# Performance work log

Measured on AMD Instinct MI355X. Metric: run time of the kernel, lower is better.

Reference implementation:

```python
import jax, jax.numpy as jnp
import numpy as np

R = 45        # num_dep_rels
L = 384       # sent_len
D = 512       # word representation dim = in_size*2
E_REL = 15    # dep_rel_emb_size
IN4 = 1024    # in_size*4
HOPS = 3
THRESH = 1e-06


def setup_inputs() -> dict:
    key = jax.random.key(0)
    ks = jax.random.split(key, 10)
    energy = jax.random.uniform(ks[0], (1, R, L, L), dtype=jnp.float32)
    word_h = jax.random.normal(ks[1], (1, L, D), dtype=jnp.float32)
    e1 = jax.random.normal(ks[2], (D,), dtype=jnp.float32)
    e2 = jax.random.normal(ks[3], (D,), dtype=jnp.float32)
    # learned params
    rel_embs = jax.random.normal(ks[4], (R, E_REL), dtype=jnp.float32)
    Wc = jax.random.normal(ks[5], (2 * D + E_REL, D), dtype=jnp.float32) * 0.02
    bc = jnp.zeros((D,), dtype=jnp.float32)
    Wk = jax.random.normal(ks[6], (HOPS, IN4, IN4), dtype=jnp.float32) * 0.02
    bk = jnp.zeros((HOPS, IN4), dtype=jnp.float32)
    Wh = jax.random.normal(ks[7], (HOPS, IN4, IN4), dtype=jnp.float32) * 0.02
    bh = jnp.zeros((HOPS, IN4), dtype=jnp.float32)
    return {"energy": energy, "word_h": word_h, "e1": e1, "e2": e2,
            "sent_len": L, "rel_embs": rel_embs, "Wc": Wc, "bc": bc,
            "Wk": Wk, "bk": bk, "Wh": Wh, "bh": bh}


def reference(energy, word_h, e1, e2, sent_len, rel_embs, Wc, bc, Wk, bk, Wh, bh):
    Ls = sent_len
    E = energy[0, :, :Ls, :Ls]                 # [R, L, L]
    marg = E.sum(axis=0)                       # [L, L] marginal energy
    # threshold back-off (try t, t/10, t/100 until some arc survives)
    m0 = marg > THRESH
    m1 = marg > THRESH * 0.1
    m2 = marg > THRESH * 0.01
    mask = jnp.where(m0.any(), m0, jnp.where(m1.any(), m1, m2))  # [L, L]

    H = word_h[0, :Ls]                         # [L, D]
    w = marg.reshape(-1)                       # [L*L] arc weights
    # rel embedding per arc: sum_r E[r,h,d] * rel_embs[r,e]
    rels = jnp.einsum('rhd,re->hde', E, rel_embs).reshape(Ls * Ls, E_REL)
    head_t = jnp.repeat(H, Ls, axis=0) * w[:, None]   # [L*L, D]
    dep_t = jnp.tile(H, (Ls, 1)) * w[:, None]         # [L*L, D]
    arc_in = jnp.concatenate([head_t, rels, dep_t], axis=1)  # [L*L, 2D+15]
    mem_bank = jax.nn.leaky_relu(arc_in @ Wc + bc)    # [L*L, D] (dropout=eval)
    maskf = mask.reshape(-1)                          # [L*L]

    # multi-hop memory attention; filtered-out arcs get zero attention weight
    inputs = jnp.concatenate([e1, e2])                # [1024]
    for i in range(HOPS):
        kv = inputs @ Wk[i] + bk[i]                   # [1024]
        k_, v_ = jnp.split(kv, 2)                     # chunk along dim 0
        k_ = jnp.tanh(k_)
        v_ = jax.nn.leaky_relu(v_)
        scores = jnp.where(maskf, mem_bank @ k_, -1e30)  # [L*L]
        dist = jax.nn.softmax(scores)
        mem_rep = dist @ mem_bank                     # [D]
        inputs = jax.nn.leaky_relu(jnp.concatenate([v_, mem_rep]) @ Wh[i] + bh[i])
    return inputs
```

## Files before the change

### kernel.cpp

```cpp
#include <hip/hip_runtime.h>
#include <hip/hip_bf16.h>
#include <cstdint>
#include <cstddef>

#define LL      147456
#define NBLK    768
#define CHB     12
#define NPACK   288

typedef __attribute__((ext_vector_type(8))) short  short8;
typedef __attribute__((ext_vector_type(4))) float  f32x4;

#define EPACK_OFF   0u
#define MARG_OFF    14155776u
#define A_OFF       14745600u
#define BTC_OFF     15532032u
#define UTGP_OFF    16318464u
#define XIN_OFF     16367616u
#define KBUF_OFF    16371712u
#define VBUF_OFF    16373760u
#define MEMREP_OFF  16375808u
#define PM_OFF      16377856u
#define PL_OFF      16380928u
#define SRAW_OFF    16384000u
#define BLKF_OFF    16973824u

#define SKIP_LD     20.0f

static __device__ __forceinline__ ushort f2bf(float x) {
  uint u = __float_as_uint(x);
  return (ushort)((u + 0x7fffu + ((u >> 16) & 1u)) >> 16);
}
static __device__ __forceinline__ float lrelu(float x) { return fmaxf(x, 0.01f * x); }

__global__ __launch_bounds__(256) void k_prep(
    const float* __restrict__ E, uint4* __restrict__ ep,
    float* __restrict__ marg, int* __restrict__ blkflags,
    const float* __restrict__ H, const float* __restrict__ Wc,
    const float* __restrict__ rel, const float* __restrict__ bc,
    float* __restrict__ A, float* __restrict__ Btc, uint4* __restrict__ Utgp) {
  __shared__ float Hs[4][512];
  __shared__ float Ps[4][512];
  __shared__ int fsh;
  int b = blockIdx.x, t = threadIdx.x;
  if (b < 192) {
    bool roleA = (b < 96);
    int g0 = (roleA ? b : b - 96) * 4;
    const float* Wcp = Wc + (size_t)(roleA ? 0 : 527) * 512;
    for (int i = t; i < 4 * 512; i += 256) Hs[i >> 9][i & 511] = H[(size_t)g0 * 512 + i];
    __syncthreads();
    int cq = t & 127, q = t >> 7;
    int c0 = cq * 4;
    f32x4 acc[4];
#pragma unroll
    for (int i = 0; i < 4; ++i) acc[i] = (f32x4){0.f, 0.f, 0.f, 0.f};
    for (int k = q * 256; k < q * 256 + 256; ++k) {
      f32x4 wv = *(const f32x4*)&Wcp[(size_t)k * 512 + c0];
#pragma unroll
      for (int i = 0; i < 4; ++i) { float hv = Hs[i][k]; acc[i] += hv * wv; }
    }
    if (q == 1) {
#pragma unroll
      for (int i = 0; i < 4; ++i) *(f32x4*)&Ps[i][c0] = acc[i];
    }
    __syncthreads();
    if (q == 0) {
#pragma unroll
      for (int i = 0; i < 4; ++i) {
        acc[i] += *(const f32x4*)&Ps[i][c0];
        if (roleA) {
          *(f32x4*)&A[(size_t)(g0 + i) * 512 + c0] = acc[i];
        } else {
#pragma unroll
          for (int j = 0; j < 4; ++j) Btc[(size_t)(c0 + j) * 384 + (g0 + i)] = acc[i][j];
        }
      }
    }
  } else if (b == 192) {
    for (int c = t; c < 512; c += 256) {
      float uv[48];
#pragma unroll
      for (int k = 0; k < 45; ++k) {
        float s = 0.f;
#pragma unroll
        for (int e = 0; e < 15; ++e) s += rel[k * 15 + e] * Wc[(size_t)(512 + e) * 512 + c];
        uv[k] = s;
      }
      uv[45] = bc[c]; uv[46] = 0.f; uv[47] = 0.f;
#pragma unroll
      for (int g = 0; g < 6; ++g) {
        uint w[4];
#pragma unroll
        for (int p = 0; p < 4; ++p)
          w[p] = (uint)f2bf(uv[g * 8 + 2 * p]) | ((uint)f2bf(uv[g * 8 + 2 * p + 1]) << 16);
        uint4 v; v.x = w[0]; v.y = w[1]; v.z = w[2]; v.w = w[3];
        Utgp[g * 512 + c] = v;
      }
    }
  } else {
    if (t == 0) fsh = 0;
    int bp = b - 193;
    size_t hd0 = (size_t)bp * 512 + 2 * t;
    float2 ev[46];
#pragma unroll
    for (int r = 0; r < 45; ++r) ev[r] = *(const float2*)&E[(size_t)r * LL + hd0];
    ev[45] = make_float2(1.0f, 1.0f);
    float s0 = 0.f, s1 = 0.f;
#pragma unroll
    for (int r = 0; r < 45; ++r) { s0 += ev[r].x; s1 += ev[r].y; }
#pragma unroll
    for (int o = 0; o < 6; ++o) {
      uint wa[4], wb[4];
#pragma unroll
      for (int p = 0; p < 4; ++p) {
        int r0 = 8 * o + 2 * p, r1 = r0 + 1;
        float a0 = (r0 < 46) ? ev[r0].x : 0.f, a1 = (r1 < 46) ? ev[r1].x : 0.f;
        float b0 = (r0 < 46) ? ev[r0].y : 0.f, b1 = (r1 < 46) ? ev[r1].y : 0.f;
        wa[p] = (uint)f2bf(a0) | ((uint)f2bf(a1) << 16);
        wb[p] = (uint)f2bf(b0) | ((uint)f2bf(b1) << 16);
      }
      uint4 va; va.x = wa[0]; va.y = wa[1]; va.z = wa[2]; va.w = wa[3];
      uint4 vb; vb.x = wb[0]; vb.y = wb[1]; vb.z = wb[2]; vb.w = wb[3];
      ep[(size_t)o * LL + hd0] = va;
      ep[(size_t)o * LL + hd0 + 1] = vb;
    }
    *(float2*)&marg[hd0] = make_float2(s0, s1);
    int f = (s0 > 1e-6f ? 1 : 0) | (s0 > 1e-7f ? 2 : 0) | (s0 > 1e-8f ? 4 : 0)
          | (s1 > 1e-6f ? 1 : 0) | (s1 > 1e-7f ? 2 : 0) | (s1 > 1e-8f ? 4 : 0);
#pragma unroll
    for (int d = 1; d < 64; d <<= 1) f |= __shfl_xor(f, d);
    __syncthreads();
    if ((t & 63) == 0) atomicOr(&fsh, f);
    __syncthreads();
    if (t == 0) blkflags[bp] = fsh;
  }
}

__global__ __launch_bounds__(256) void k_gemv(const float* __restrict__ W, const float* __restrict__ bias,
                                              const float* __restrict__ xA, const float* __restrict__ xB,
                                              float* __restrict__ outA, float* __restrict__ outB,
                                              float* __restrict__ out2, int mode) {
  __shared__ float xs[1024];
  __shared__ float red[8][32];
  int t = threadIdx.x;
  for (int i = t; i < 1024; i += 256) xs[i] = (i < 512) ? xA[i] : xB[i - 512];
  __syncthreads();
  int jj = t & 31, kq = t >> 5;
  int j = blockIdx.x * 32 + jj;
  float acc = 0.f;
#pragma unroll 8
  for (int k = kq * 128; k < kq * 128 + 128; ++k) acc = fmaf(xs[k], W[(size_t)k * 1024 + j], acc);
  red[kq][jj] = acc;
  __syncthreads();
  if (kq == 0) {
    float s = bias[j];
#pragma unroll
    for (int q = 0; q < 8; ++q) s += red[q][jj];
    if (mode == 0) {
      if (j < 512) outA[j] = tanhf(s);
      else outB[j - 512] = lrelu(s);
    } else {
      float rv = lrelu(s);
      outA[j] = rv;
      if (out2) out2[j] = rv;
    }
  }
}

__global__ __launch_bounds__(256, 3) void k_scores(
    const uint4* __restrict__ ep, const float* __restrict__ marg,
    const float* __restrict__ A, const float* __restrict__ Btc,
    const uint4* __restrict__ Utgp, const int* __restrict__ blkflags,
    const float* __restrict__ kvec,
    float* __restrict__ pm, float* __restrict__ pl, float* __restrict__ sraw,
    float* __restrict__ memrep) {
  __shared__ __align__(16) uint4 uthF[6 * 512];
  __shared__ float sbuf[CHB * 16];
  __shared__ float redw[8];
  __shared__ int fsh;
  int t = threadIdx.x, b = blockIdx.x;
  int dbt = b >> 5, hg = b & 31;
  int dbase = dbt * 16, h0 = hg * CHB;
  int lane = t & 63, wid = t >> 6;
  int l15 = lane & 15, qq = lane >> 4;

  if (b == 0) { memrep[t] = 0.f; memrep[t + 256] = 0.f; }
  if (t == 0) fsh = 0;
  for (int i = t; i < 6 * 512; i += 256) uthF[i] = Utgp[i];
  int f = 0;
  for (int i = t; i < NPACK; i += 256) f |= blkflags[i];
#pragma unroll
  for (int d = 1; d < 64; d <<= 1) f |= __shfl_xor(f, d);

  const short8 zero8 = (short8){0, 0, 0, 0, 0, 0, 0, 0};
  short8 a0[3], a1[3];
  f32x4 wq[3];
#pragma unroll
  for (int k3 = 0; k3 < 3; ++k3) {
    int h = h0 + wid * 3 + k3;
    int hda = h * 384 + dbase + l15;
    uint4 r0 = ep[(size_t)qq * LL + hda];
    a0[k3] = *(short8*)&r0;
    if (qq < 2) { uint4 r1 = ep[(size_t)(4 + qq) * LL + hda]; a1[k3] = *(short8*)&r1; }
    else a1[k3] = zero8;
    wq[k3] = *(const f32x4*)&marg[h * 384 + dbase + qq * 4];
  }
  __syncthreads();
  if ((t & 63) == 0) atomicOr(&fsh, f);

  float sp[3][4];
#pragma unroll
  for (int k3 = 0; k3 < 3; ++k3)
#pragma unroll
    for (int j = 0; j < 4; ++j) sp[k3][j] = 0.f;

  for (int half = 0; half < 2; ++half) {
    float kreg[16];
#pragma unroll
    for (int tt = 0; tt < 16; ++tt) kreg[tt] = kvec[half * 256 + tt * 16 + l15];
#pragma unroll 4
    for (int tt = 0; tt < 16; ++tt) {
      int c = half * 256 + tt * 16 + l15;
      short8 b0 = *(short8*)&uthF[qq * 512 + c];
      short8 b1 = (qq < 2) ? *(short8*)&uthF[(4 + qq) * 512 + c] : zero8;
      f32x4 btv = *(const f32x4*)&Btc[(size_t)c * 384 + dbase + qq * 4];
      const float* Ap = &A[(size_t)(h0 + wid * 3) * 512 + c];
      float av[3]; av[0] = Ap[0]; av[1] = Ap[512]; av[2] = Ap[1024];
#pragma unroll
      for (int k3 = 0; k3 < 3; ++k3) {
        f32x4 cc = (f32x4){0.f, 0.f, 0.f, 0.f};
        cc = __builtin_amdgcn_mfma_f32_16x16x32_bf16(a0[k3], b0, cc, 0, 0, 0);
        cc = __builtin_amdgcn_mfma_f32_16x16x32_bf16(a1[k3], b1, cc, 0, 0, 0);
        float aw = av[k3];
        float x0 = cc[0] + wq[k3][0] * (aw + btv[0]); float mb0 = fmaxf(x0, 0.01f * x0);
        float x1 = cc[1] + wq[k3][1] * (aw + btv[1]); float mb1 = fmaxf(x1, 0.01f * x1);
        float x2 = cc[2] + wq[k3][2] * (aw + btv[2]); float mb2 = fmaxf(x2, 0.01f * x2);
        float x3 = cc[3] + wq[k3][3] * (aw + btv[3]); float mb3 = fmaxf(x3, 0.01f * x3);
        sp[k3][0] = fmaf(mb0, kreg[tt], sp[k3][0]);
        sp[k3][1] = fmaf(mb1, kreg[tt], sp[k3][1]);
        sp[k3][2] = fmaf(mb2, kreg[tt], sp[k3][2]);
        sp[k3][3] = fmaf(mb3, kreg[tt], sp[k3][3]);
      }
    }
  }
#pragma unroll
  for (int k3 = 0; k3 < 3; ++k3)
#pragma unroll
    for (int j = 0; j < 4; ++j) {
#pragma unroll
      for (int d = 1; d < 16; d <<= 1) sp[k3][j] += __shfl_xor(sp[k3][j], d);
    }
  __syncthreads();
  float thr = (fsh & 1) ? 1e-6f : ((fsh & 2) ? 1e-7f : 1e-8f);
  if (l15 == 0) {
#pragma unroll
    for (int k3 = 0; k3 < 3; ++k3) {
      int base = (wid * 3 + k3) * 16 + qq * 4;
#pragma unroll
      for (int j = 0; j < 4; ++j)
        sbuf[base + j] = (wq[k3][j] > thr) ? sp[k3][j] : -1e30f;
    }
  }
  __syncthreads();
  float s = (t < CHB * 16) ? sbuf[t] : -1e30f;
  float m = s;
#pragma unroll
  for (int d = 1; d < 64; d <<= 1) m = fmaxf(m, __shfl_xor(m, d));
  if (lane == 0) redw[wid] = m;
  __syncthreads();
  float mloc = fmaxf(fmaxf(redw[0], redw[1]), fmaxf(redw[2], redw[3]));
  float e = (t < CHB * 16) ? __expf(s - mloc) : 0.f;
#pragma unroll
  for (int d = 1; d < 64; d <<= 1) e += __shfl_xor(e, d);
  if (lane == 0) redw[4 + wid] = e;
  if (t < CHB * 16) sraw[(size_t)b * 192 + t] = s;
  __syncthreads();
  if (t == 0) { pm[b] = mloc; pl[b] = redw[4] + redw[5] + redw[6] + redw[7]; }
}

__global__ __launch_bounds__(256, 3) void k_pv(
    const uint4* __restrict__ ep, const float* __restrict__ marg,
    const float* __restrict__ A, const float* __restrict__ Btc,
    const uint4* __restrict__ Utgp, const float* __restrict__ pm,
    const float* __restrict__ pl, const float* __restrict__ sraw,
    float* __restrict__ memrep) {
  __shared__ __align__(16) uint4 uthF[6 * 512];
  __shared__ float pbuf[CHB * 16];
  __shared__ float paccs[256];
  __shared__ float redm[8];
  int t = threadIdx.x, b = blockIdx.x;
  int lane = t & 63, wid = t >> 6;

  float m = -1e30f;
  for (int i = t; i < NBLK; i += 256) m = fmaxf(m, pm[i]);
#pragma unroll
  for (int d = 1; d < 64; d <<= 1) m = fmaxf(m, __shfl_xor(m, d));
  if (lane == 0) redm[wid] = m;
  __syncthreads();
  float M = fmaxf(fmaxf(redm[0], redm[1]), fmaxf(redm[2], redm[3]));
  float ls = 0.f;
  for (int i = t; i < NBLK; i += 256) {
    float d = pm[i] - M;
    if (!(d < -SKIP_LD)) ls += __expf(d) * pl[i];
  }
#pragma unroll
  for (int d = 1; d < 64; d <<= 1) ls += __shfl_xor(ls, d);
  if (lane == 0) redm[4 + wid] = ls;
  __syncthreads();
  float L = redm[4] + redm[5] + redm[6] + redm[7];
  float pmb = pm[b];
  if (pmb - M < -SKIP_LD) return;
  float w = __expf(pmb - M) / L;

  int dbt = b >> 5, hg = b & 31;
  int dbase = dbt * 16, h0 = hg * CHB;
  int l15 = lane & 15, qq = lane >> 4;

  for (int i = t; i < 6 * 512; i += 256) uthF[i] = Utgp[i];
  if (t < CHB * 16) pbuf[t] = __expf(sraw[(size_t)b * 192 + t] - pmb);

  const short8 zero8 = (short8){0, 0, 0, 0, 0, 0, 0, 0};
  short8 a0[3], a1[3];
  f32x4 wq[3];
#pragma unroll
  for (int k3 = 0; k3 < 3; ++k3) {
    int h = h0 + wid * 3 + k3;
    int hda = h * 384 + dbase + l15;
    uint4 r0 = ep[(size_t)qq * LL + hda];
    a0[k3] = *(short8*)&r0;
    if (qq < 2) { uint4 r1 = ep[(size_t)(4 + qq) * LL + hda]; a1[k3] = *(short8*)&r1; }
    else a1[k3] = zero8;
    wq[k3] = *(const f32x4*)&marg[h * 384 + dbase + qq * 4];
  }
  __syncthreads();

  float pvw[3][4];
#pragma unroll
  for (int k3 = 0; k3 < 3; ++k3)
#pragma unroll
    for (int j = 0; j < 4; ++j)
      pvw[k3][j] = pbuf[(wid * 3 + k3) * 16 + qq * 4 + j];

  for (int half = 0; half < 2; ++half) {
    paccs[t] = 0.f;
    __syncthreads();
#pragma unroll 4
    for (int tt = 0; tt < 16; ++tt) {
      int c = half * 256 + tt * 16 + l15;
      short8 b0 = *(short8*)&uthF[qq * 512 + c];
      short8 b1 = (qq < 2) ? *(short8*)&uthF[(4 + qq) * 512 + c] : zero8;
      f32x4 btv = *(const f32x4*)&Btc[(size_t)c * 384 + dbase + qq * 4];
      const float* Ap = &A[(size_t)(h0 + wid * 3) * 512 + c];
      float av[3]; av[0] = Ap[0]; av[1] = Ap[512]; av[2] = Ap[1024];
      float acc_t = 0.f;
#pragma unroll
      for (int k3 = 0; k3 < 3; ++k3) {
        f32x4 cc = (f32x4){0.f, 0.f, 0.f, 0.f};
        cc = __builtin_amdgcn_mfma_f32_16x16x32_bf16(a0[k3], b0, cc, 0, 0, 0);
        cc = __builtin_amdgcn_mfma_f32_16x16x32_bf16(a1[k3], b1, cc, 0, 0, 0);
        float aw = av[k3];
        float x0 = cc[0] + wq[k3][0] * (aw + btv[0]); float mb0 = fmaxf(x0, 0.01f * x0);
        float x1 = cc[1] + wq[k3][1] * (aw + btv[1]); float mb1 = fmaxf(x1, 0.01f * x1);
        float x2 = cc[2] + wq[k3][2] * (aw + btv[2]); float mb2 = fmaxf(x2, 0.01f * x2);
        float x3 = cc[3] + wq[k3][3] * (aw + btv[3]); float mb3 = fmaxf(x3, 0.01f * x3);
        acc_t = fmaf(pvw[k3][0], mb0, fmaf(pvw[k3][1], mb1,
                fmaf(pvw[k3][2], mb2, fmaf(pvw[k3][3], mb3, acc_t))));
      }
      acc_t += __shfl_xor(acc_t, 16);
      acc_t += __shfl_xor(acc_t, 32);
      if (lane < 16) atomicAdd(&paccs[tt * 16 + l15], acc_t);
    }
    __syncthreads();
    atomicAdd(&memrep[half * 256 + t], paccs[t] * w);
    __syncthreads();
  }
}

extern "C" void kernel_launch(void* const* d_in, const int* in_sizes, int n_in,
                              void* d_out, int out_size, void* d_ws, size_t ws_size,
                              hipStream_t stream) {
  const float* E   = (const float*)d_in[0];
  const float* H   = (const float*)d_in[1];
  const float* e1  = (const float*)d_in[2];
  const float* e2  = (const float*)d_in[3];
  const float* rel = (const float*)d_in[5];
  const float* Wc  = (const float*)d_in[6];
  const float* bc  = (const float*)d_in[7];
  const float* Wk  = (const float*)d_in[8];
  const float* bk  = (const float*)d_in[9];
  const float* Wh  = (const float*)d_in[10];
  const float* bh  = (const float*)d_in[11];

  char* ws = (char*)d_ws;
  uint4*  ep     = (uint4*)(ws + EPACK_OFF);
  float*  marg   = (float*)(ws + MARG_OFF);
  float*  Abuf   = (float*)(ws + A_OFF);
  float*  Btc    = (float*)(ws + BTC_OFF);
  uint4*  Utgp   = (uint4*)(ws + UTGP_OFF);
  float*  xin    = (float*)(ws + XIN_OFF);
  float*  kbuf   = (float*)(ws + KBUF_OFF);
  float*  vbuf   = (float*)(ws + VBUF_OFF);
  float*  memrep = (float*)(ws + MEMREP_OFF);
  float*  pm     = (float*)(ws + PM_OFF);
  float*  pl     = (float*)(ws + PL_OFF);
  float*  sraw   = (float*)(ws + SRAW_OFF);
  int*    blkf   = (int*)(ws + BLKF_OFF);

  k_prep<<<481, 256, 0, stream>>>(E, ep, marg, blkf, H, Wc, rel, bc, Abuf, Btc, Utgp);

  for (int hop = 0; hop < 3; ++hop) {
    const float* Wki = Wk + (size_t)hop * 1024 * 1024;
    const float* bki = bk + (size_t)hop * 1024;
    const float* Whi = Wh + (size_t)hop * 1024 * 1024;
    const float* bhi = bh + (size_t)hop * 1024;
    k_gemv<<<32, 256, 0, stream>>>(Wki, bki, hop == 0 ? e1 : xin,
                                   hop == 0 ? e2 : xin + 512, kbuf, vbuf,
                                   (float*)nullptr, 0);
    k_scores<<<NBLK, 256, 0, stream>>>(ep, marg, Abuf, Btc, Utgp, blkf, kbuf,
                                       pm, pl, sraw, memrep);
    k_pv<<<NBLK, 256, 0, stream>>>(ep, marg, Abuf, Btc, Utgp, pm, pl, sraw, memrep);
    k_gemv<<<32, 256, 0, stream>>>(Whi, bhi, vbuf, memrep, xin, (float*)nullptr,
                                   hop == 2 ? (float*)d_out : (float*)nullptr, 1);
  }
}
```

Measured before the change: 205.3 us.

## Fuse score and PV passes with block-local softmax, combine partials in output GEMV

The separate scores and PV kernels are merged into one kernel. Each block computes its local max and exp-weights, then does the weighted mem_bank accumulation using the local max and writes an unscaled 512-float partial per block. The Wh GEMV kernel now rescales and sums these partials with the global max and denominator, skipping blocks far below the max, before its matvec. Both GEMVs move from 32 to 64 blocks. This saves one kernel launch per hop and avoids regenerating operand fragments. In exchange it adds a 768x512 partial buffer that every GEMV block re-reduces redundantly, and PV work is no longer skipped for negligible blocks.

```diff
diff --git a/kernel.cpp b/kernel.cpp
--- a/kernel.cpp
+++ b/kernel.cpp
@@ -19,11 +19,10 @@
 #define XIN_OFF     16367616u
 #define KBUF_OFF    16371712u
 #define VBUF_OFF    16373760u
-#define MEMREP_OFF  16375808u
 #define PM_OFF      16377856u
 #define PL_OFF      16380928u
-#define SRAW_OFF    16384000u
-#define BLKF_OFF    16973824u
+#define PACC_OFF    16384000u
+#define BLKF_OFF    17956864u
 
 #define SKIP_LD     20.0f
 
@@ -138,45 +137,38 @@
 
 __global__ __launch_bounds__(256) void k_gemv(const float* __restrict__ W, const float* __restrict__ bias,
                                               const float* __restrict__ xA, const float* __restrict__ xB,
-                                              float* __restrict__ outA, float* __restrict__ outB,
-                                              float* __restrict__ out2, int mode) {
+                                              float* __restrict__ kbuf, float* __restrict__ vbuf) {
   __shared__ float xs[1024];
-  __shared__ float red[8][32];
+  __shared__ float red[256];
   int t = threadIdx.x;
   for (int i = t; i < 1024; i += 256) xs[i] = (i < 512) ? xA[i] : xB[i - 512];
   __syncthreads();
-  int jj = t & 31, kq = t >> 5;
-  int j = blockIdx.x * 32 + jj;
+  int jj = t & 15, kq = t >> 4;
+  int j = blockIdx.x * 16 + jj;
   float acc = 0.f;
 #pragma unroll 8
-  for (int k = kq * 128; k < kq * 128 + 128; ++k) acc = fmaf(xs[k], W[(size_t)k * 1024 + j], acc);
-  red[kq][jj] = acc;
+  for (int k = kq * 64; k < kq * 64 + 64; ++k) acc = fmaf(xs[k], W[(size_t)k * 1024 + j], acc);
+  red[kq * 16 + jj] = acc;
   __syncthreads();
   if (kq == 0) {
     float s = bias[j];
 #pragma unroll
-    for (int q = 0; q < 8; ++q) s += red[q][jj];
-    if (mode == 0) {
-      if (j < 512) outA[j] = tanhf(s);
-      else outB[j - 512] = lrelu(s);
-    } else {
-      float rv = lrelu(s);
-      outA[j] = rv;
-      if (out2) out2[j] = rv;
-    }
-  }
-}
-
-__global__ __launch_bounds__(256, 3) void k_scores(
+    for (int q = 0; q < 16; ++q) s += red[q * 16 + jj];
+    if (j < 512) kbuf[j] = tanhf(s);
+    else vbuf[j - 512] = lrelu(s);
+  }
+}
+
+__global__ __launch_bounds__(256, 3) void k_fused(
     const uint4* __restrict__ ep, const float* __restrict__ marg,
     const float* __restrict__ A, const float* __restrict__ Btc,
     const uint4* __restrict__ Utgp, const int* __restrict__ blkflags,
     const float* __restrict__ kvec,
-    float* __restrict__ pm, float* __restrict__ pl, float* __restrict__ sraw,
-    float* __restrict__ memrep) {
+    float* __restrict__ pm, float* __restrict__ pl, float* __restrict__ pacc) {
   __shared__ __align__(16) uint4 uthF[6 * 512];
   __shared__ float sbuf[CHB * 16];
   __shared__ float redw[8];
+  __shared__ float paccs[256];
   __shared__ int fsh;
   int t = threadIdx.x, b = blockIdx.x;
   int dbt = b >> 5, hg = b & 31;
@@ -184,7 +176,6 @@
   int lane = t & 63, wid = t >> 6;
   int l15 = lane & 15, qq = lane >> 4;
 
-  if (b == 0) { memrep[t] = 0.f; memrep[t + 256] = 0.f; }
   if (t == 0) fsh = 0;
   for (int i = t; i < 6 * 512; i += 256) uthF[i] = Utgp[i];
   int f = 0;
@@ -262,84 +253,27 @@
     }
   }
   __syncthreads();
-  float s = (t < CHB * 16) ? sbuf[t] : -1e30f;
-  float m = s;
+
+  float sv = (t < CHB * 16) ? sbuf[t] : -1e30f;
+  float m = sv;
 #pragma unroll
   for (int d = 1; d < 64; d <<= 1) m = fmaxf(m, __shfl_xor(m, d));
   if (lane == 0) redw[wid] = m;
   __syncthreads();
   float mloc = fmaxf(fmaxf(redw[0], redw[1]), fmaxf(redw[2], redw[3]));
-  float e = (t < CHB * 16) ? __expf(s - mloc) : 0.f;
+  float e = (t < CHB * 16) ? __expf(sv - mloc) : 0.f;
 #pragma unroll
   for (int d = 1; d < 64; d <<= 1) e += __shfl_xor(e, d);
   if (lane == 0) redw[4 + wid] = e;
-  if (t < CHB * 16) sraw[(size_t)b * 192 + t] = s;
   __syncthreads();
   if (t == 0) { pm[b] = mloc; pl[b] = redw[4] + redw[5] + redw[6] + redw[7]; }
-}
-
-__global__ __launch_bounds__(256, 3) void k_pv(
-    const uint4* __restrict__ ep, const float* __restrict__ marg,
-    const float* __restrict__ A, const float* __restrict__ Btc,
-    const uint4* __restrict__ Utgp, const float* __restrict__ pm,
-    const float* __restrict__ pl, const float* __restrict__ sraw,
-    float* __restrict__ memrep) {
-  __shared__ __align__(16) uint4 uthF[6 * 512];
-  __shared__ float pbuf[CHB * 16];
-  __shared__ float paccs[256];
-  __shared__ float redm[8];
-  int t = threadIdx.x, b = blockIdx.x;
-  int lane = t & 63, wid = t >> 6;
-
-  float m = -1e30f;
-  for (int i = t; i < NBLK; i += 256) m = fmaxf(m, pm[i]);
-#pragma unroll
-  for (int d = 1; d < 64; d <<= 1) m = fmaxf(m, __shfl_xor(m, d));
-  if (lane == 0) redm[wid] = m;
-  __syncthreads();
-  float M = fmaxf(fmaxf(redm[0], redm[1]), fmaxf(redm[2], redm[3]));
-  float ls = 0.f;
-  for (int i = t; i < NBLK; i += 256) {
-    float d = pm[i] - M;
-    if (!(d < -SKIP_LD)) ls += __expf(d) * pl[i];
-  }
-#pragma unroll
-  for (int d = 1; d < 64; d <<= 1) ls += __shfl_xor(ls, d);
-  if (lane == 0) redm[4 + wid] = ls;
-  __syncthreads();
-  float L = redm[4] + redm[5] + redm[6] + redm[7];
-  float pmb = pm[b];
-  if (pmb - M < -SKIP_LD) return;
-  float w = __expf(pmb - M) / L;
-
-  int dbt = b >> 5, hg = b & 31;
-  int dbase = dbt * 16, h0 = hg * CHB;
-  int l15 = lane & 15, qq = lane >> 4;
-
-  for (int i = t; i < 6 * 512; i += 256) uthF[i] = Utgp[i];
-  if (t < CHB * 16) pbuf[t] = __expf(sraw[(size_t)b * 192 + t] - pmb);
-
-  const short8 zero8 = (short8){0, 0, 0, 0, 0, 0, 0, 0};
-  short8 a0[3], a1[3];
-  f32x4 wq[3];
-#pragma unroll
-  for (int k3 = 0; k3 < 3; ++k3) {
-    int h = h0 + wid * 3 + k3;
-    int hda = h * 384 + dbase + l15;
-    uint4 r0 = ep[(size_t)qq * LL + hda];
-    a0[k3] = *(short8*)&r0;
-    if (qq < 2) { uint4 r1 = ep[(size_t)(4 + qq) * LL + hda]; a1[k3] = *(short8*)&r1; }
-    else a1[k3] = zero8;
-    wq[k3] = *(const f32x4*)&marg[h * 384 + dbase + qq * 4];
-  }
-  __syncthreads();
 
   float pvw[3][4];
 #pragma unroll
   for (int k3 = 0; k3 < 3; ++k3)
 #pragma unroll
     for (int j = 0; j < 4; ++j)
-      pvw[k3][j] = pbuf[(wid * 3 + k3) * 16 + qq * 4 + j];
+      pvw[k3][j] = __expf(sbuf[(wid * 3 + k3) * 16 + qq * 4 + j] - mloc);
 
   for (int half = 0; half < 2; ++half) {
     paccs[t] = 0.f;
@@ -371,8 +305,87 @@
       if (lane < 16) atomicAdd(&paccs[tt * 16 + l15], acc_t);
     }
     __syncthreads();
-    atomicAdd(&memrep[half * 256 + t], paccs[t] * w);
-    __syncthreads();
+    pacc[(size_t)b * 512 + half * 256 + t] = paccs[t];
+    __syncthreads();
+  }
+}
+
+__global__ __launch_bounds__(256) void k_gemvc(
+    const float* __restrict__ W, const float* __restrict__ bias,
+    const float* __restrict__ vbuf, const float* __restrict__ pm,
+    const float* __restrict__ pl, const float* __restrict__ pacc,
+    float* __restrict__ outA, float* __restrict__ out2) {
+  __shared__ float xs[1024];
+  __shared__ float sc[NBLK];
+  __shared__ int slist[NBLK];
+  __shared__ int scnt_sh;
+  __shared__ float redm[8];
+  __shared__ float red[256];
+  int t = threadIdx.x;
+  int lane = t & 63, wid = t >> 6;
+
+  float m = -1e30f;
+  for (int i = t; i < NBLK; i += 256) m = fmaxf(m, pm[i]);
+#pragma unroll
+  for (int d = 1; d < 64; d <<= 1) m = fmaxf(m, __shfl_xor(m, d));
+  if (lane == 0) redm[wid] = m;
+  __syncthreads();
+  float M = fmaxf(fmaxf(redm[0], redm[1]), fmaxf(redm[2], redm[3]));
+  float ls = 0.f;
+  for (int i = t; i < NBLK; i += 256) {
+    float d = pm[i] - M;
+    float e = (d < -SKIP_LD) ? 0.f : __expf(d);
+    sc[i] = e;
+    ls += e * pl[i];
+  }
+#pragma unroll
+  for (int d = 1; d < 64; d <<= 1) ls += __shfl_xor(ls, d);
+  if (lane == 0) redm[4 + wid] = ls;
+  __syncthreads();
+  float L = redm[4] + redm[5] + redm[6] + redm[7];
+
+  if (wid == 0) {
+    int cnt = 0;
+#pragma unroll
+    for (int rnd = 0; rnd < NBLK / 64; ++rnd) {
+      int bb = rnd * 64 + lane;
+      bool p = sc[bb] > 0.f;
+      unsigned long long mask = __ballot(p);
+      int off = __popcll(mask & ((1ull << lane) - 1ull));
+      if (p) slist[cnt + off] = bb;
+      cnt += __popcll(mask);
+    }
+    if (lane == 0) scnt_sh = cnt;
+  }
+  __syncthreads();
+  int S = scnt_sh;
+  for (int c = t; c < 512; c += 256) xs[c] = vbuf[c];
+#pragma unroll
+  for (int half = 0; half < 2; ++half) {
+    int c = t + half * 256;
+    float s = 0.f;
+    for (int k = 0; k < S; ++k) {
+      int bb = slist[k];
+      s += pacc[(size_t)bb * 512 + c] * sc[bb];
+    }
+    xs[512 + c] = s / L;
+  }
+  __syncthreads();
+
+  int jj = t & 15, kq = t >> 4;
+  int j = blockIdx.x * 16 + jj;
+  float acc = 0.f;
+#pragma unroll 8
+  for (int k = kq * 64; k < kq * 64 + 64; ++k) acc = fmaf(xs[k], W[(size_t)k * 1024 + j], acc);
+  red[kq * 16 + jj] = acc;
+  __syncthreads();
+  if (kq == 0) {
+    float s = bias[j];
+#pragma unroll
+    for (int q = 0; q < 16; ++q) s += red[q * 16 + jj];
+    float rv = lrelu(s);
+    outA[j] = rv;
+    if (out2) out2[j] = rv;
   }
 }
 
@@ -400,10 +413,9 @@
   float*  xin    = (float*)(ws + XIN_OFF);
   float*  kbuf   = (float*)(ws + KBUF_OFF);
   float*  vbuf   = (float*)(ws + VBUF_OFF);
-  float*  memrep = (float*)(ws + MEMREP_OFF);
   float*  pm     = (float*)(ws + PM_OFF);
   float*  pl     = (float*)(ws + PL_OFF);
-  float*  sraw   = (float*)(ws + SRAW_OFF);
+  float*  pacc   = (float*)(ws + PACC_OFF);
   int*    blkf   = (int*)(ws + BLKF_OFF);
 
   k_prep<<<481, 256, 0, stream>>>(E, ep, marg, blkf, H, Wc, rel, bc, Abuf, Btc, Utgp);
@@ -413,13 +425,11 @@
     const float* bki = bk + (size_t)hop * 1024;
     const float* Whi = Wh + (size_t)hop * 1024 * 1024;
     const float* bhi = bh + (size_t)hop * 1024;
-    k_gemv<<<32, 256, 0, stream>>>(Wki, bki, hop == 0 ? e1 : xin,
-                                   hop == 0 ? e2 : xin + 512, kbuf, vbuf,
-                                   (float*)nullptr, 0);
-    k_scores<<<NBLK, 256, 0, stream>>>(ep, marg, Abuf, Btc, Utgp, blkf, kbuf,
-                                       pm, pl, sraw, memrep);
-    k_pv<<<NBLK, 256, 0, stream>>>(ep, marg, Abuf, Btc, Utgp, pm, pl, sraw, memrep);
-    k_gemv<<<32, 256, 0, stream>>>(Whi, bhi, vbuf, memrep, xin, (float*)nullptr,
-                                   hop == 2 ? (float*)d_out : (float*)nullptr, 1);
-  }
-}
+    k_gemv<<<64, 256, 0, stream>>>(Wki, bki, hop == 0 ? e1 : xin,
+                                   hop == 0 ? e2 : xin + 512, kbuf, vbuf);
+    k_fused<<<NBLK, 256, 0, stream>>>(ep, marg, Abuf, Btc, Utgp, blkf, kbuf,
+                                      pm, pl, pacc);
+    k_gemvc<<<64, 256, 0, stream>>>(Whi, bhi, vbuf, pm, pl, pacc, xin,
+                                    hop == 2 ? (float*)d_out : (float*)nullptr);
+  }
+}
```

Result: faster. 196.3 us (-4.4%).
